# Performance work log

Measured on AMD Instinct MI355X. Metric: run time of the kernel, lower is better.

## Reference

```python
import jax, jax.numpy as jnp
import numpy as np
from jax import lax

GRID = 50
T_DIM = 1
Y_DIM = GRID * GRID
R_DIM = 128
Z_DIM = 64
H_DIM = 128
C_CONV = 32


def _conv(x, w, b):
    # x: [N, Cin, H, W], w: [Cout, Cin, 3, 3]
    y = lax.conv_general_dilated(x, w, (1, 1), 'SAME',
                                 dimension_numbers=('NCHW', 'OIHW', 'NCHW'))
    return y + b[None, :, None, None]


def setup_inputs() -> dict:
    key = jax.random.key(0)
    ks = jax.random.split(key, 24)
    B, NC, NT = 16, 64, 128
    s = lambda k, sh, f: (jax.random.normal(k, sh, jnp.float32) * f)
    inp = {
        'x_context': jax.random.normal(ks[0], (B, NC, T_DIM), jnp.float32),
        'y_context': jax.random.normal(ks[1], (B, NC, Y_DIM), jnp.float32),
        'x_target': jax.random.normal(ks[2], (B, NT, T_DIM), jnp.float32),
        'eps': jax.random.normal(ks[3], (B, Z_DIM), jnp.float32),
        # CNN encoder (Net)
        'w1': s(ks[4], (C_CONV, 2, 3, 3), 0.2), 'b1': jnp.zeros((C_CONV,), jnp.float32),
        'w2': s(ks[5], (C_CONV, C_CONV, 3, 3), 0.1), 'b2': jnp.zeros((C_CONV,), jnp.float32),
        'We1': s(ks[6], (C_CONV + T_DIM, H_DIM), 0.1), 'be1': jnp.zeros((H_DIM,), jnp.float32),
        'We2': s(ks[7], (H_DIM, R_DIM), 0.1), 'be2': jnp.zeros((R_DIM,), jnp.float32),
        # MuSigmaEncoder
        'Wh': s(ks[8], (R_DIM, H_DIM), 0.1), 'bh': jnp.zeros((H_DIM,), jnp.float32),
        'Wmu': s(ks[9], (H_DIM, Z_DIM), 0.1), 'bmu': jnp.zeros((Z_DIM,), jnp.float32),
        'Wsig': s(ks[10], (H_DIM, Z_DIM), 0.1), 'bsig': jnp.zeros((Z_DIM,), jnp.float32),
        # Decoder
        'Wd1': s(ks[11], (T_DIM + Z_DIM, H_DIM), 0.1), 'bd1': jnp.zeros((H_DIM,), jnp.float32),
        'Wd2': s(ks[12], (H_DIM, H_DIM), 0.1), 'bd2': jnp.zeros((H_DIM,), jnp.float32),
        'Wdmu': s(ks[13], (H_DIM, Y_DIM), 0.05), 'bdmu': jnp.zeros((Y_DIM,), jnp.float32),
        'Wdsig': s(ks[14], (H_DIM, Y_DIM), 0.05), 'bdsig': jnp.zeros((Y_DIM,), jnp.float32),
    }
    return inp


def _xy_to_mu_sigma(x, y, p):
    B, N, _ = x.shape
    x_flat = x.reshape(B * N, T_DIM)                      # [BN, 1]
    y_grid = y.reshape(B * N, 1, GRID, GRID)              # [BN,1,50,50]
    # broadcast of x value over the grid (replaces per-sample Python loop)
    x_grid = jnp.broadcast_to(x_flat[:, 0, None, None, None], (B * N, 1, GRID, GRID))
    xy_grid = jnp.concatenate([y_grid, x_grid], axis=1)   # [BN,2,50,50]
    h = jax.nn.relu(_conv(xy_grid, p['w1'], p['b1']))
    h = jax.nn.relu(_conv(h, p['w2'], p['b2']))
    pooled = h.mean(axis=(2, 3))                          # [BN, C_CONV]
    feat = jnp.concatenate([pooled, x_flat], axis=-1)     # [BN, C_CONV+1]
    r_i = jnp.dot(jax.nn.relu(jnp.dot(feat, p['We1']) + p['be1']), p['We2']) + p['be2']
    r = r_i.reshape(B, N, R_DIM).mean(axis=1)             # aggregate over points
    hr = jax.nn.relu(jnp.dot(r, p['Wh']) + p['bh'])
    mu = jnp.dot(hr, p['Wmu']) + p['bmu']
    sigma = 0.1 + 0.9 * jax.nn.sigmoid(jnp.dot(hr, p['Wsig']) + p['bsig'])
    return mu, sigma


def _decode(x_target, z, p):
    B, M, _ = x_target.shape
    z_rep = jnp.broadcast_to(z[:, None, :], (B, M, Z_DIM))
    xz = jnp.concatenate([x_target, z_rep], axis=-1)      # [B,M,1+Z]
    h = jax.nn.relu(jnp.dot(xz, p['Wd1']) + p['bd1'])
    h = jax.nn.relu(jnp.dot(h, p['Wd2']) + p['bd2'])
    y_mu = jnp.dot(h, p['Wdmu']) + p['bdmu']
    y_sigma = 0.1 + 0.9 * jax.nn.softplus(jnp.dot(h, p['Wdsig']) + p['bdsig'])
    return y_mu, y_sigma


def reference(x_context, y_context, x_target, eps,
              w1, b1, w2, b2, We1, be1, We2, be2,
              Wh, bh, Wmu, bmu, Wsig, bsig,
              Wd1, bd1, Wd2, bd2, Wdmu, bdmu, Wdsig, bdsig):
    p = dict(w1=w1, b1=b1, w2=w2, b2=b2, We1=We1, be1=be1, We2=We2, be2=be2,
             Wh=Wh, bh=bh, Wmu=Wmu, bmu=bmu, Wsig=Wsig, bsig=bsig,
             Wd1=Wd1, bd1=bd1, Wd2=Wd2, bd2=bd2, Wdmu=Wdmu, bdmu=bdmu,
             Wdsig=Wdsig, bdsig=bdsig)
    mu_c, sigma_c = _xy_to_mu_sigma(x_context, y_context, p)
    z = mu_c + sigma_c * eps                               # rsample (reparameterized)
    y_mu, y_sigma = _decode(x_target, z, p)
    return y_mu, y_sigma, mu_c, sigma_c
```

## Files before the change

### kernel.cpp

```cpp
#include <hip/hip_runtime.h>

#define GRID_N   50
#define YDIM     2500
#define BATCH    16
#define NCTX     64
#define NTGT     128
#define BN       1024
#define RDIM     128
#define ZDIM     64
#define HDIM     128
#define CCONV    32
#define NSTRIP   5
#define STRIPROWS 10

typedef __attribute__((ext_vector_type(8))) short  s8v;
typedef __attribute__((ext_vector_type(4))) float  f4v;
typedef __attribute__((ext_vector_type(4))) unsigned int u4v;

__device__ __forceinline__ unsigned short f2bf(float f) {
    unsigned int u = __float_as_uint(f);
    u += 0x7FFFu + ((u >> 16) & 1u);
    return (unsigned short)(u >> 16);
}
__device__ __forceinline__ unsigned int cvtpk(float lo, float hi) {
    unsigned int r;
    asm("v_cvt_pk_bf16_f32 %0, %1, %2" : "=v"(r) : "v"(lo), "v"(hi));
    return r;
}


#define PLB   39936
#define PY    2
#define PX    738
#define P1    1490
#define DUP   2228
#define OFFT  48848
#define REDB  48912
#define SMEMB 49424

__global__ void k_pack_w(const float* __restrict__ w1, const float* __restrict__ b1,
                         const float* __restrict__ w2,
                         unsigned short* __restrict__ w2p, unsigned short* __restrict__ w1p)
{
    int t = threadIdx.x;
    int l = t & 63, qq = t >> 6;
    int cout_lo = l & 15, cb = (l >> 4) & 3;
    for (int e = qq; e < 18; e += 4) {
        int tap = e >> 1, ntt = e & 1;
        int cout = ntt * 16 + cout_lo;
        unsigned int pk[4];
#pragma unroll
        for (int g = 0; g < 4; ++g) {
            int cin0 = cb * 8 + 2 * g;
            unsigned int lo = f2bf(w2[(cout * 32 + cin0) * 9 + tap]);
            unsigned int hi = f2bf(w2[(cout * 32 + cin0 + 1) * 9 + tap]);
            pk[g] = lo | (hi << 16);
        }
        uint4 o; o.x = pk[0]; o.y = pk[1]; o.z = pk[2]; o.w = pk[3];
        *(uint4*)&w2p[((tap * 2 + ntt) * 64 + l) * 8] = o;
    }
    if (t < 128) {
        int ct = t >> 6, lane = t & 63;
        int c = ct * 16 + (lane & 15), q2 = lane >> 4;
        const signed char kmap[32] = {0,1,3,4,6,7,16,17,  2,-1,5,-1,8,-1,18,-1,
                                      19,20,21,-1,22,23,24,-1, 32,-1,-1,-1,-1,-1,-1,-1};
        unsigned short v8[8];
#pragma unroll
        for (int j = 0; j < 8; ++j) {
            int km = kmap[q2 * 8 + j];
            float v = 0.f;
            if (km == 32) v = b1[c];
            else if (km >= 16) v = w1[(c * 2 + 1) * 9 + (km - 16)];
            else if (km >= 0) v = w1[(c * 2 + 0) * 9 + km];
            v8[j] = f2bf(v);
        }
        uint4 o;
        o.x = (unsigned)v8[0] | ((unsigned)v8[1] << 16);
        o.y = (unsigned)v8[2] | ((unsigned)v8[3] << 16);
        o.z = (unsigned)v8[4] | ((unsigned)v8[5] << 16);
        o.w = (unsigned)v8[6] | ((unsigned)v8[7] << 16);
        *(uint4*)&w1p[(ct * 64 + lane) * 8] = o;
    }
}

__global__ void k_pack_wd(const float* __restrict__ Wmu, const float* __restrict__ Wsg,
                          unsigned short* __restrict__ wdp)
{
    int nt = blockIdx.x;
    int which = blockIdx.y;
    const float* W = which ? Wsg : Wmu;
    unsigned short* outp = wdp + (size_t)which * (157 * 4 * 64 * 8);
    int t = threadIdx.x;
    int l = t & 63, ks = t >> 6;
    int n = nt * 16 + (l & 15);
    int kbase = ks * 32 + ((l >> 4) & 3) * 8;
    unsigned int pk[4];
#pragma unroll
    for (int g = 0; g < 4; ++g) {
        float f0 = (n < 2500) ? W[(kbase + 2 * g) * 2500 + n] : 0.f;
        float f1 = (n < 2500) ? W[(kbase + 2 * g + 1) * 2500 + n] : 0.f;
        pk[g] = (unsigned int)f2bf(f0) | ((unsigned int)f2bf(f1) << 16);
    }
    uint4 o; o.x = pk[0]; o.y = pk[1]; o.z = pk[2]; o.w = pk[3];
    *(uint4*)&outp[((nt * 4 + ks) * 64 + l) * 8] = o;
}

__global__ __launch_bounds__(256, 3) void k_conv(
    const float* __restrict__ xc, const float* __restrict__ yc,
    const unsigned short* __restrict__ w1p, const unsigned short* __restrict__ w2p,
    const float* __restrict__ b2, float* __restrict__ part)
{
    __shared__ __align__(16) char smem[SMEMB];
    unsigned short* pl = (unsigned short*)(smem + PLB);
    int* offtab = (int*)(smem + OFFT);
    float* redbuf = (float*)(smem + REDB);

    const int t = threadIdx.x, lane = t & 63, w = t >> 6;
    const int l15 = lane & 15, q = lane >> 4;
    const int par = lane & 1;
    const int blk = blockIdx.x, s = blk / NSTRIP, strip = blk - s * NSTRIP;
    const int r0 = strip * STRIPROWS;

    const float xv = xc[s];
    const unsigned short xbf = f2bf(xv);
    const float b2v0 = b2[l15], b2v1 = b2[16 + l15];

    if (t < 16) {
        const int btab[16] = {1, 53, 105, 737,   3, 55, 107, 739,
                              789, 791, 841, 843,  P1, P1, P1, P1};
        offtab[t] = btab[t];
    }
    for (int e = t; e < 736; e += 256) {
        unsigned ry = ((unsigned)(e * 1261)) >> 16;
        int ycol = e - (int)ry * 52;
        int gy = r0 - 2 + (int)ry, gc = ycol - 1;
        bool inb = ((unsigned)gy < 50u) && ((unsigned)gc < 50u);
        unsigned short yb = 0, xb = 0;
        if (inb) { yb = f2bf(yc[s * YDIM + gy * 50 + gc]); xb = xbf; }
        int s0 = PY + e, s1 = PX + e, s2 = P1 + e;
        pl[s0] = yb; if (s0 >= 3) pl[DUP + s0 - 3] = yb;
        pl[s1] = xb; pl[DUP + s1 - 3] = xb;
        pl[s2] = 0x3F80; pl[DUP + s2 - 3] = 0x3F80;
    }
    __syncthreads();

    s8v w1f[2];
#pragma unroll
    for (int ct = 0; ct < 2; ++ct)
        w1f[ct] = *(const s8v*)&w1p[(ct * 64 + lane) * 8];
    int boff[4];
#pragma unroll
    for (int i = 0; i < 4; ++i) {
        int B = offtab[q * 4 + i];
        int pr = (B + lane) & 1;
        boff[i] = PLB + ((pr ? (DUP - 3 + B) : B) << 1);
    }
    const f4v zf = {0.f, 0.f, 0.f, 0.f};
    for (int mt = w; mt < 39; mt += 4) {
        int m = mt * 16 + l15;
        int mb = m * 2;
        unsigned g0 = *(const unsigned*)(smem + boff[0] + mb);
        unsigned g1 = *(const unsigned*)(smem + boff[1] + mb);
        unsigned g2 = *(const unsigned*)(smem + boff[2] + mb);
        unsigned g3 = *(const unsigned*)(smem + boff[3] + mb);
        u4v gg = {g0, g1, g2, g3};
        s8v af = __builtin_bit_cast(s8v, gg);
        f4v c0 = __builtin_amdgcn_mfma_f32_16x16x32_bf16(w1f[0], af, zf, 0, 0, 0);
        f4v c1 = __builtin_amdgcn_mfma_f32_16x16x32_bf16(w1f[1], af, zf, 0, 0, 0);
        unsigned mr = ((unsigned)(m * 1261)) >> 16;
        int mc = m - (int)mr * 52;
        int gy = r0 - 1 + (int)mr;
        bool valid = ((unsigned)(mc - 1) < 50u) && ((unsigned)gy < 50u);
        unsigned p0 = cvtpk(fmaxf(c0[0], 0.f), fmaxf(c0[1], 0.f));
        unsigned p1 = cvtpk(fmaxf(c0[2], 0.f), fmaxf(c0[3], 0.f));
        unsigned p2 = cvtpk(fmaxf(c1[0], 0.f), fmaxf(c1[1], 0.f));
        unsigned p3 = cvtpk(fmaxf(c1[2], 0.f), fmaxf(c1[3], 0.f));
        if (!valid) { p0 = 0u; p1 = 0u; p2 = 0u; p3 = 0u; }
        int rrow = m >> 1;
        int modd4 = (m & 1) << 2;
        int r7 = rrow & 7;
        char* base = smem + (rrow << 7) + ((q & 1) << 3);
        int s0w = ((modd4 | (q >> 1)) ^ r7) << 4;
        int s1w = ((modd4 | (2 + (q >> 1))) ^ r7) << 4;
        *(uint2*)(base + s0w) = make_uint2(p0, p1);
        *(uint2*)(base + s1w) = make_uint2(p2, p3);
    }
    __syncthreads();

    f4v acc[8][2];
#pragma unroll
    for (int i = 0; i < 8; ++i) { acc[i][0] = zf; acc[i][1] = zf; }
    int u_[8], up_[8];
#pragma unroll
    for (int tt = 0; tt < 8; ++tt) {
        int m2 = (w * 8 + tt) * 16 + l15;
        unsigned orr = ((unsigned)(m2 * 1311)) >> 16;
        int pc = m2 + 2 * (int)orr;
        u_[tt] = pc >> 1;
        up_[tt] = u_[tt] + par;
    }
    const int oq  = (par << 2) | q;
    const int oqx = ((par ^ 1) << 2) | q;
#pragma unroll
    for (int tp = 0; tp < 9; ++tp) {
        const int ky = tp / 3, kx = tp % 3;
        s8v b0 = *(const s8v*)&w2p[((tp * 2 + 0) * 64 + lane) * 8];
        s8v b1 = *(const s8v*)&w2p[((tp * 2 + 1) * 64 + lane) * 8];
#pragma unroll
        for (int tt = 0; tt < 8; ++tt) {
            int r = (kx == 1 ? up_[tt] : u_[tt]) + 26 * ky + (kx == 2 ? 1 : 0);
            int so = ((kx == 1 ? oqx : oq) ^ (r & 7)) << 4;
            s8v a = *(const s8v*)(smem + (r << 7) + so);
            acc[tt][0] = __builtin_amdgcn_mfma_f32_16x16x32_bf16(a, b0, acc[tt][0], 0, 0, 0);
            acc[tt][1] = __builtin_amdgcn_mfma_f32_16x16x32_bf16(a, b1, acc[tt][1], 0, 0, 0);
        }
    }
    float ps0 = 0.f, ps1 = 0.f;
#pragma unroll
    for (int tt = 0; tt < 8; ++tt) {
        int mbase = (w * 8 + tt) * 16 + q * 4;
#pragma unroll
        for (int r = 0; r < 4; ++r) {
            if (mbase + r < 500) {
                ps0 += fmaxf(acc[tt][0][r] + b2v0, 0.f);
                ps1 += fmaxf(acc[tt][1][r] + b2v1, 0.f);
            }
        }
    }
    ps0 += __shfl_xor(ps0, 16); ps0 += __shfl_xor(ps0, 32);
    ps1 += __shfl_xor(ps1, 16); ps1 += __shfl_xor(ps1, 32);
    if (lane < 16) {
        redbuf[w * 32 + l15] = ps0;
        redbuf[w * 32 + 16 + l15] = ps1;
    }
    __syncthreads();
    if (t < 32)
        part[(s * NSTRIP + strip) * 32 + t] =
            redbuf[t] + redbuf[32 + t] + redbuf[64 + t] + redbuf[96 + t];
}

__global__ void k_enc(const float* __restrict__ part, const float* __restrict__ xc,
                      const float* __restrict__ We1, const float* __restrict__ be1,
                      const float* __restrict__ We2, const float* __restrict__ be2,
                      float* __restrict__ r_i)
{
    __shared__ float feat[33];
    __shared__ float h[128];
    int s = blockIdx.x, j = threadIdx.x;
    if (j < 32) {
        float v = 0.f;
#pragma unroll
        for (int st = 0; st < NSTRIP; ++st) v += part[(s * NSTRIP + st) * 32 + j];
        feat[j] = v * (1.f / 2500.f);
    }
    if (j == 0) feat[32] = xc[s];
    __syncthreads();
    float a = be1[j];
#pragma unroll 4
    for (int k = 0; k < 33; ++k) a = fmaf(feat[k], We1[k * 128 + j], a);
    h[j] = fmaxf(a, 0.f);
    __syncthreads();
    float r = be2[j];
#pragma unroll 8
    for (int k = 0; k < 128; ++k) r = fmaf(h[k], We2[k * 128 + j], r);
    r_i[s * 128 + j] = r;
}

__global__ void k_ms(const float* __restrict__ r_i,
                     const float* __restrict__ Wh, const float* __restrict__ bh,
                     const float* __restrict__ Wmu, const float* __restrict__ bmu,
                     const float* __restrict__ Wsig, const float* __restrict__ bsig,
                     const float* __restrict__ eps, float* __restrict__ out,
                     float* __restrict__ zbuf)
{
    __shared__ float r[128], hr[128], tmp[2][128];
    int b = blockIdx.x, t = threadIdx.x;
    int j = t & 127, g = t >> 7;
    float acc = 0.f;
#pragma unroll 4
    for (int i = g; i < NCTX; i += 2) acc += r_i[(b * NCTX + i) * 128 + j];
    tmp[g][j] = acc;
    __syncthreads();
    if (g == 0) r[j] = (tmp[0][j] + tmp[1][j]) * (1.f / 64.f);
    __syncthreads();
    float a = (g == 0) ? bh[j] : 0.f;
#pragma unroll 8
    for (int k = g * 64; k < g * 64 + 64; ++k) a = fmaf(r[k], Wh[k * 128 + j], a);
    tmp[g][j] = a;
    __syncthreads();
    if (g == 0) hr[j] = fmaxf(tmp[0][j] + tmp[1][j], 0.f);
    __syncthreads();
    if (j < 64) {
        float m = (g == 0) ? bmu[j] : 0.f, sg = (g == 0) ? bsig[j] : 0.f;
#pragma unroll 8
        for (int k = g * 64; k < g * 64 + 64; ++k) {
            m  = fmaf(hr[k], Wmu[k * 64 + j], m);
            sg = fmaf(hr[k], Wsig[k * 64 + j], sg);
        }
        tmp[g][j] = m; tmp[g][64 + j] = sg;
    }
    __syncthreads();
    if (t < 64) {
        float m  = tmp[0][t] + tmp[1][t];
        float sg = tmp[0][64 + t] + tmp[1][64 + t];
        float sig = 0.1f + 0.9f / (1.f + expf(-sg));
        out[10240000 + b * 64 + t] = m;
        out[10241024 + b * 64 + t] = sig;
        zbuf[b * 64 + t] = m + sig * eps[b * 64 + t];
    }
}

__global__ __launch_bounds__(256) void k_dec1(
    const float* __restrict__ xt, const float* __restrict__ zbuf,
    const float* __restrict__ Wd1, const float* __restrict__ bd1,
    const float* __restrict__ Wd2, const float* __restrict__ bd2,
    unsigned short* __restrict__ h2d)
{
    __shared__ float zsh[64];
    __shared__ float vsh[2][128];
    __shared__ float h1sh[4][128];
    int t = threadIdx.x;
    int j = t & 127, g = t >> 7;
    int r0 = blockIdx.x * 4;
    int b = r0 >> 7;
    if (t < 64) zsh[t] = zbuf[b * 64 + t];
    __syncthreads();
    float v = (g == 0) ? bd1[j] : 0.f;
#pragma unroll 8
    for (int k = g * 32; k < g * 32 + 32; ++k)
        v = fmaf(zsh[k], Wd1[(1 + k) * 128 + j], v);
    vsh[g][j] = v;
    __syncthreads();
    float vv = vsh[0][j] + vsh[1][j];
    float w0 = Wd1[j];
    int ra = r0 + g * 2;
    float x0 = xt[ra], x1 = xt[ra + 1];
    h1sh[g * 2][j]     = fmaxf(fmaf(x0, w0, vv), 0.f);
    h1sh[g * 2 + 1][j] = fmaxf(fmaf(x1, w0, vv), 0.f);
    __syncthreads();
    float bd2j = bd2[j];
    float a0 = bd2j, a1 = bd2j;
#pragma unroll 8
    for (int k = 0; k < 128; ++k) {
        float wv = Wd2[k * 128 + j];
        a0 = fmaf(h1sh[g * 2][k], wv, a0);
        a1 = fmaf(h1sh[g * 2 + 1][k], wv, a1);
    }
    h2d[(size_t)ra * 128 + j]       = f2bf(fmaxf(a0, 0.f));
    h2d[(size_t)(ra + 1) * 128 + j] = f2bf(fmaxf(a1, 0.f));
}

__global__ __launch_bounds__(256) void k_gemm(
    const unsigned short* __restrict__ h2d, const unsigned short* __restrict__ wdp,
    const float* __restrict__ bdmu, const float* __restrict__ bdsg,
    float* __restrict__ out)
{
    __shared__ __align__(16) unsigned short Al[64 * 128];
    int t = threadIdx.x, lane = t & 63, w = t >> 6;
    int m0 = blockIdx.x * 64;
    int which = blockIdx.z;
#pragma unroll
    for (int i = 0; i < 4; ++i) {
        int g = t + i * 256;
        int row = g >> 4, bk = g & 15;
        uint4 v = *(const uint4*)&h2d[(size_t)(m0 + row) * 128 + bk * 8];
        *(uint4*)&Al[row * 128 + ((bk ^ (row & 7)) << 3)] = v;
    }
    __syncthreads();
    int nt = blockIdx.y * 4 + w;
    if (nt < 157) {
        const unsigned short* wp = wdp + (size_t)which * (157 * 4 * 64 * 8);
        s8v bfr[4];
#pragma unroll
        for (int ks = 0; ks < 4; ++ks)
            bfr[ks] = *(const s8v*)&wp[((nt * 4 + ks) * 64 + lane) * 8];
        f4v acc[4];
        {
            f4v zf = {0.f, 0.f, 0.f, 0.f};
#pragma unroll
            for (int mt = 0; mt < 4; ++mt) acc[mt] = zf;
        }
        int lcol = lane & 15, lq = lane >> 4;
#pragma unroll
        for (int mt = 0; mt < 4; ++mt) {
            int mrow = mt * 16 + lcol;
#pragma unroll
            for (int ks = 0; ks < 4; ++ks) {
                int bk = ks * 4 + lq;
                s8v a = *(const s8v*)&Al[mrow * 128 + ((bk ^ (mrow & 7)) << 3)];
                acc[mt] = __builtin_amdgcn_mfma_f32_16x16x32_bf16(a, bfr[ks], acc[mt], 0, 0, 0);
            }
        }
        int col = nt * 16 + lcol;
        if (col < 2500) {
            const float* bp = which ? bdsg : bdmu;
            float bv = bp[col];
            size_t zoff = (size_t)which * 5120000;
#pragma unroll
            for (int mt = 0; mt < 4; ++mt)
#pragma unroll
                for (int r = 0; r < 4; ++r) {
                    int row = m0 + mt * 16 + lq * 4 + r;
                    float vv = acc[mt][r] + bv;
                    if (which) {
                        float sp = fmaxf(vv, 0.f) + log1pf(expf(-fabsf(vv)));
                        vv = 0.1f + 0.9f * sp;
                    }
                    out[zoff + (size_t)row * 2500 + col] = vv;
                }
        }
    }
}

extern "C" void kernel_launch(void* const* d_in, const int* in_sizes, int n_in,
                              void* d_out, int out_size, void* d_ws, size_t ws_size,
                              hipStream_t stream)
{
    const float* xc   = (const float*)d_in[0];
    const float* yc   = (const float*)d_in[1];
    const float* xt   = (const float*)d_in[2];
    const float* eps  = (const float*)d_in[3];
    const float* w1   = (const float*)d_in[4];
    const float* b1   = (const float*)d_in[5];
    const float* w2   = (const float*)d_in[6];
    const float* b2   = (const float*)d_in[7];
    const float* We1  = (const float*)d_in[8];
    const float* be1  = (const float*)d_in[9];
    const float* We2  = (const float*)d_in[10];
    const float* be2  = (const float*)d_in[11];
    const float* Wh   = (const float*)d_in[12];
    const float* bh   = (const float*)d_in[13];
    const float* Wmu  = (const float*)d_in[14];
    const float* bmu  = (const float*)d_in[15];
    const float* Wsig = (const float*)d_in[16];
    const float* bsig = (const float*)d_in[17];
    const float* Wd1  = (const float*)d_in[18];
    const float* bd1  = (const float*)d_in[19];
    const float* Wd2  = (const float*)d_in[20];
    const float* bd2  = (const float*)d_in[21];
    const float* Wdmu = (const float*)d_in[22];
    const float* bdmu = (const float*)d_in[23];
    const float* Wdsg = (const float*)d_in[24];
    const float* bdsg = (const float*)d_in[25];

    float* out = (float*)d_out;
    char* wsb  = (char*)d_ws;
    unsigned short* w2p = (unsigned short*)(wsb + 0);
    unsigned short* wdp = (unsigned short*)(wsb + 18432);
    float* part = (float*)(wsb + 1304576);
    float* r_i  = (float*)(wsb + 1959936);
    float* zbuf = (float*)(wsb + 2484224);
    unsigned short* h2d = (unsigned short*)(wsb + 2488320);
    unsigned short* w1p = (unsigned short*)(wsb + 3012608);

    hipLaunchKernelGGL(k_pack_w, dim3(1), dim3(256), 0, stream, w1, b1, w2, w2p, w1p);
    hipLaunchKernelGGL(k_pack_wd, dim3(157, 2), dim3(256), 0, stream, Wdmu, Wdsg, wdp);
    hipLaunchKernelGGL(k_conv, dim3(BN * NSTRIP), dim3(256), 0, stream,
                       xc, yc, w1p, w2p, b2, part);
    hipLaunchKernelGGL(k_enc, dim3(BN), dim3(128), 0, stream,
                       part, xc, We1, be1, We2, be2, r_i);
    hipLaunchKernelGGL(k_ms, dim3(BATCH), dim3(256), 0, stream,
                       r_i, Wh, bh, Wmu, bmu, Wsig, bsig, eps, out, zbuf);
    hipLaunchKernelGGL(k_dec1, dim3(512), dim3(256), 0, stream,
                       xt, zbuf, Wd1, bd1, Wd2, bd2, h2d);
    hipLaunchKernelGGL(k_gemm, dim3(32, 40, 2), dim3(256), 0, stream,
                       h2d, wdp, bdmu, bdsg, out);
}
```

Baseline: 134.6 us.

## Shrink conv LDS footprint, merge pack kernels, and fuse mu/sigma GEMM launches

Overlays the conv1 staging plane onto the conv1-output buffer so k_conv uses less LDS, allowing four blocks per CU instead of three. The boundary conv1 tiles are computed before a barrier and written after it. The offset table moves into registers, the conv2 phase gets a raised wave priority, and the reduction mask is simplified. The two weight-packing kernels merge into one launch, and the decoder GEMM handles mu and sigma in the same block, halving the grid. The input permutation for w2 packing also changes to match a new 16-byte LDS write layout. The LDS aliasing adds an extra barrier and risks read/write hazards.

```diff
diff --git a/kernel.cpp b/kernel.cpp
--- a/kernel.cpp
+++ b/kernel.cpp
@@ -29,68 +29,68 @@
 }
 
 
-#define PLB   39936
+#define PLB   31024
 #define PY    2
 #define PX    738
 #define P1    1490
 #define DUP   2228
-#define OFFT  48848
-#define REDB  48912
-#define SMEMB 49424
-
-__global__ void k_pack_w(const float* __restrict__ w1, const float* __restrict__ b1,
-                         const float* __restrict__ w2,
-                         unsigned short* __restrict__ w2p, unsigned short* __restrict__ w1p)
+#define SMEMB 39936
+
+
+__global__ void k_pack(const float* __restrict__ w1, const float* __restrict__ b1,
+                       const float* __restrict__ w2,
+                       unsigned short* __restrict__ w2p, unsigned short* __restrict__ w1p,
+                       const float* __restrict__ Wmu, const float* __restrict__ Wsg,
+                       unsigned short* __restrict__ wdp)
 {
     int t = threadIdx.x;
-    int l = t & 63, qq = t >> 6;
-    int cout_lo = l & 15, cb = (l >> 4) & 3;
-    for (int e = qq; e < 18; e += 4) {
-        int tap = e >> 1, ntt = e & 1;
-        int cout = ntt * 16 + cout_lo;
-        unsigned int pk[4];
-#pragma unroll
-        for (int g = 0; g < 4; ++g) {
-            int cin0 = cb * 8 + 2 * g;
-            unsigned int lo = f2bf(w2[(cout * 32 + cin0) * 9 + tap]);
-            unsigned int hi = f2bf(w2[(cout * 32 + cin0 + 1) * 9 + tap]);
-            pk[g] = lo | (hi << 16);
-        }
-        uint4 o; o.x = pk[0]; o.y = pk[1]; o.z = pk[2]; o.w = pk[3];
-        *(uint4*)&w2p[((tap * 2 + ntt) * 64 + l) * 8] = o;
-    }
-    if (t < 128) {
-        int ct = t >> 6, lane = t & 63;
-        int c = ct * 16 + (lane & 15), q2 = lane >> 4;
-        const signed char kmap[32] = {0,1,3,4,6,7,16,17,  2,-1,5,-1,8,-1,18,-1,
-                                      19,20,21,-1,22,23,24,-1, 32,-1,-1,-1,-1,-1,-1,-1};
-        unsigned short v8[8];
-#pragma unroll
-        for (int j = 0; j < 8; ++j) {
-            int km = kmap[q2 * 8 + j];
-            float v = 0.f;
-            if (km == 32) v = b1[c];
-            else if (km >= 16) v = w1[(c * 2 + 1) * 9 + (km - 16)];
-            else if (km >= 0) v = w1[(c * 2 + 0) * 9 + km];
-            v8[j] = f2bf(v);
-        }
-        uint4 o;
-        o.x = (unsigned)v8[0] | ((unsigned)v8[1] << 16);
-        o.y = (unsigned)v8[2] | ((unsigned)v8[3] << 16);
-        o.z = (unsigned)v8[4] | ((unsigned)v8[5] << 16);
-        o.w = (unsigned)v8[6] | ((unsigned)v8[7] << 16);
-        *(uint4*)&w1p[(ct * 64 + lane) * 8] = o;
-    }
-}
-
-__global__ void k_pack_wd(const float* __restrict__ Wmu, const float* __restrict__ Wsg,
-                          unsigned short* __restrict__ wdp)
-{
+    if (blockIdx.y == 2) {
+        if (blockIdx.x != 0) return;
+        int l = t & 63, qq = t >> 6;
+        int cout_lo = l & 15, cb = (l >> 4) & 3;
+        for (int e = qq; e < 18; e += 4) {
+            int tap = e >> 1, ntt = e & 1;
+            int cout = ntt * 16 + cout_lo;
+            unsigned int pk[4];
+#pragma unroll
+            for (int g = 0; g < 4; ++g) {
+                int jj = 2 * g;
+                int cinL = (jj < 4) ? (cb * 4 + jj) : (16 + cb * 4 + (jj - 4));
+                unsigned int lo = f2bf(w2[(cout * 32 + cinL) * 9 + tap]);
+                unsigned int hi = f2bf(w2[(cout * 32 + cinL + 1) * 9 + tap]);
+                pk[g] = lo | (hi << 16);
+            }
+            uint4 o; o.x = pk[0]; o.y = pk[1]; o.z = pk[2]; o.w = pk[3];
+            *(uint4*)&w2p[((tap * 2 + ntt) * 64 + l) * 8] = o;
+        }
+        if (t < 128) {
+            int ct = t >> 6, lane = t & 63;
+            int c = ct * 16 + (lane & 15), q2 = lane >> 4;
+            const signed char kmap[32] = {0,1,3,4,6,7,16,17,  2,-1,5,-1,8,-1,18,-1,
+                                          19,20,21,-1,22,23,24,-1, 32,-1,-1,-1,-1,-1,-1,-1};
+            unsigned short v8[8];
+#pragma unroll
+            for (int j = 0; j < 8; ++j) {
+                int km = kmap[q2 * 8 + j];
+                float v = 0.f;
+                if (km == 32) v = b1[c];
+                else if (km >= 16) v = w1[(c * 2 + 1) * 9 + (km - 16)];
+                else if (km >= 0) v = w1[(c * 2 + 0) * 9 + km];
+                v8[j] = f2bf(v);
+            }
+            uint4 o;
+            o.x = (unsigned)v8[0] | ((unsigned)v8[1] << 16);
+            o.y = (unsigned)v8[2] | ((unsigned)v8[3] << 16);
+            o.z = (unsigned)v8[4] | ((unsigned)v8[5] << 16);
+            o.w = (unsigned)v8[6] | ((unsigned)v8[7] << 16);
+            *(uint4*)&w1p[(ct * 64 + lane) * 8] = o;
+        }
+        return;
+    }
     int nt = blockIdx.x;
     int which = blockIdx.y;
     const float* W = which ? Wsg : Wmu;
     unsigned short* outp = wdp + (size_t)which * (157 * 4 * 64 * 8);
-    int t = threadIdx.x;
     int l = t & 63, ks = t >> 6;
     int n = nt * 16 + (l & 15);
     int kbase = ks * 32 + ((l >> 4) & 3) * 8;
@@ -105,15 +105,14 @@
     *(uint4*)&outp[((nt * 4 + ks) * 64 + l) * 8] = o;
 }
 
-__global__ __launch_bounds__(256, 3) void k_conv(
+__global__ __launch_bounds__(256, 4) void k_conv(
     const float* __restrict__ xc, const float* __restrict__ yc,
     const unsigned short* __restrict__ w1p, const unsigned short* __restrict__ w2p,
     const float* __restrict__ b2, float* __restrict__ part)
 {
     __shared__ __align__(16) char smem[SMEMB];
     unsigned short* pl = (unsigned short*)(smem + PLB);
-    int* offtab = (int*)(smem + OFFT);
-    float* redbuf = (float*)(smem + REDB);
+    float* redbuf = (float*)smem;
 
     const int t = threadIdx.x, lane = t & 63, w = t >> 6;
     const int l15 = lane & 15, q = lane >> 4;
@@ -125,11 +124,6 @@
     const unsigned short xbf = f2bf(xv);
     const float b2v0 = b2[l15], b2v1 = b2[16 + l15];
 
-    if (t < 16) {
-        const int btab[16] = {1, 53, 105, 737,   3, 55, 107, 739,
-                              789, 791, 841, 843,  P1, P1, P1, P1};
-        offtab[t] = btab[t];
-    }
     for (int e = t; e < 736; e += 256) {
         unsigned ry = ((unsigned)(e * 1261)) >> 16;
         int ycol = e - (int)ry * 52;
@@ -142,27 +136,32 @@
         pl[s1] = xb; pl[DUP + s1 - 3] = xb;
         pl[s2] = 0x3F80; pl[DUP + s2 - 3] = 0x3F80;
     }
-    __syncthreads();
 
     s8v w1f[2];
 #pragma unroll
     for (int ct = 0; ct < 2; ++ct)
         w1f[ct] = *(const s8v*)&w1p[(ct * 64 + lane) * 8];
-    int boff[4];
-#pragma unroll
-    for (int i = 0; i < 4; ++i) {
-        int B = offtab[q * 4 + i];
+
+    int B0 = (q == 0) ? 1 : (q == 1) ? 3 : (q == 2) ? 789 : P1;
+    int B1 = (q < 2) ? (B0 + 52)  : ((q == 2) ? 791 : P1);
+    int B2 = (q < 2) ? (B0 + 104) : ((q == 2) ? 841 : P1);
+    int B3 = (q < 2) ? (B0 + 736) : ((q == 2) ? 843 : P1);
+    auto mkoff = [&](int B) {
         int pr = (B + lane) & 1;
-        boff[i] = PLB + ((pr ? (DUP - 3 + B) : B) << 1);
-    }
+        return PLB + ((pr ? (DUP - 3 + B) : B) << 1);
+    };
+    const int bo0 = mkoff(B0), bo1 = mkoff(B1), bo2 = mkoff(B2), bo3 = mkoff(B3);
+
+    __syncthreads();
+
     const f4v zf = {0.f, 0.f, 0.f, 0.f};
-    for (int mt = w; mt < 39; mt += 4) {
+    auto do_tile = [&](int mt) -> uint4 {
         int m = mt * 16 + l15;
         int mb = m * 2;
-        unsigned g0 = *(const unsigned*)(smem + boff[0] + mb);
-        unsigned g1 = *(const unsigned*)(smem + boff[1] + mb);
-        unsigned g2 = *(const unsigned*)(smem + boff[2] + mb);
-        unsigned g3 = *(const unsigned*)(smem + boff[3] + mb);
+        unsigned g0 = *(const unsigned*)(smem + bo0 + mb);
+        unsigned g1 = *(const unsigned*)(smem + bo1 + mb);
+        unsigned g2 = *(const unsigned*)(smem + bo2 + mb);
+        unsigned g3 = *(const unsigned*)(smem + bo3 + mb);
         u4v gg = {g0, g1, g2, g3};
         s8v af = __builtin_bit_cast(s8v, gg);
         f4v c0 = __builtin_amdgcn_mfma_f32_16x16x32_bf16(w1f[0], af, zf, 0, 0, 0);
@@ -176,14 +175,34 @@
         unsigned p2 = cvtpk(fmaxf(c1[0], 0.f), fmaxf(c1[1], 0.f));
         unsigned p3 = cvtpk(fmaxf(c1[2], 0.f), fmaxf(c1[3], 0.f));
         if (!valid) { p0 = 0u; p1 = 0u; p2 = 0u; p3 = 0u; }
+        return make_uint4(p0, p1, p2, p3);
+    };
+    auto wr_tile = [&](int mt, uint4 v) {
+        int m = mt * 16 + l15;
         int rrow = m >> 1;
-        int modd4 = (m & 1) << 2;
-        int r7 = rrow & 7;
-        char* base = smem + (rrow << 7) + ((q & 1) << 3);
-        int s0w = ((modd4 | (q >> 1)) ^ r7) << 4;
-        int s1w = ((modd4 | (2 + (q >> 1))) ^ r7) << 4;
-        *(uint2*)(base + s0w) = make_uint2(p0, p1);
-        *(uint2*)(base + s1w) = make_uint2(p2, p3);
+        int slot = (((m & 1) << 2) | q) ^ (rrow & 7);
+        *(uint4*)(smem + (rrow << 7) + (slot << 4)) = v;
+    };
+
+#pragma unroll
+    for (int it = 0; it < 8; ++it) {
+        int mt = w + it * 4;
+        if (mt <= 29) {
+            uint4 v = do_tile(mt);
+            wr_tile(mt, v);
+        }
+    }
+    {
+        int mt0 = (w >= 2) ? (28 + w) : (32 + w);
+        uint4 hA = do_tile(mt0);
+        uint4 hB = do_tile(mt0 + 4);
+        uint4 hC = make_uint4(0u, 0u, 0u, 0u);
+        bool third = (w == 2);
+        if (third) hC = do_tile(38);
+        __syncthreads();
+        wr_tile(mt0, hA);
+        wr_tile(mt0 + 4, hB);
+        if (third) wr_tile(38, hC);
     }
     __syncthreads();
 
@@ -196,11 +215,14 @@
         int m2 = (w * 8 + tt) * 16 + l15;
         unsigned orr = ((unsigned)(m2 * 1311)) >> 16;
         int pc = m2 + 2 * (int)orr;
-        u_[tt] = pc >> 1;
-        up_[tt] = u_[tt] + par;
+        int u = pc >> 1;
+        u = (u > 258) ? 258 : u;
+        u_[tt] = u;
+        up_[tt] = u + par;
     }
     const int oq  = (par << 2) | q;
     const int oqx = ((par ^ 1) << 2) | q;
+    __builtin_amdgcn_s_setprio(1);
 #pragma unroll
     for (int tp = 0; tp < 9; ++tp) {
         const int ky = tp / 3, kx = tp % 3;
@@ -215,20 +237,32 @@
             acc[tt][1] = __builtin_amdgcn_mfma_f32_16x16x32_bf16(a, b1, acc[tt][1], 0, 0, 0);
         }
     }
+    __builtin_amdgcn_s_setprio(0);
+
     float ps0 = 0.f, ps1 = 0.f;
 #pragma unroll
     for (int tt = 0; tt < 8; ++tt) {
-        int mbase = (w * 8 + tt) * 16 + q * 4;
-#pragma unroll
-        for (int r = 0; r < 4; ++r) {
-            if (mbase + r < 500) {
+        int tile = w * 8 + tt;
+        if (tile != 31) {
+#pragma unroll
+            for (int r = 0; r < 4; ++r) {
                 ps0 += fmaxf(acc[tt][0][r] + b2v0, 0.f);
                 ps1 += fmaxf(acc[tt][1][r] + b2v1, 0.f);
             }
+        } else {
+            int mbase = tile * 16 + q * 4;
+#pragma unroll
+            for (int r = 0; r < 4; ++r) {
+                if (mbase + r < 500) {
+                    ps0 += fmaxf(acc[tt][0][r] + b2v0, 0.f);
+                    ps1 += fmaxf(acc[tt][1][r] + b2v1, 0.f);
+                }
+            }
         }
     }
     ps0 += __shfl_xor(ps0, 16); ps0 += __shfl_xor(ps0, 32);
     ps1 += __shfl_xor(ps1, 16); ps1 += __shfl_xor(ps1, 32);
+    __syncthreads();
     if (lane < 16) {
         redbuf[w * 32 + l15] = ps0;
         redbuf[w * 32 + 16 + l15] = ps1;
@@ -358,7 +392,6 @@
     __shared__ __align__(16) unsigned short Al[64 * 128];
     int t = threadIdx.x, lane = t & 63, w = t >> 6;
     int m0 = blockIdx.x * 64;
-    int which = blockIdx.z;
 #pragma unroll
     for (int i = 0; i < 4; ++i) {
         int g = t + i * 256;
@@ -369,45 +402,48 @@
     __syncthreads();
     int nt = blockIdx.y * 4 + w;
     if (nt < 157) {
-        const unsigned short* wp = wdp + (size_t)which * (157 * 4 * 64 * 8);
-        s8v bfr[4];
-#pragma unroll
-        for (int ks = 0; ks < 4; ++ks)
-            bfr[ks] = *(const s8v*)&wp[((nt * 4 + ks) * 64 + lane) * 8];
-        f4v acc[4];
-        {
-            f4v zf = {0.f, 0.f, 0.f, 0.f};
-#pragma unroll
-            for (int mt = 0; mt < 4; ++mt) acc[mt] = zf;
-        }
         int lcol = lane & 15, lq = lane >> 4;
-#pragma unroll
-        for (int mt = 0; mt < 4; ++mt) {
-            int mrow = mt * 16 + lcol;
-#pragma unroll
-            for (int ks = 0; ks < 4; ++ks) {
-                int bk = ks * 4 + lq;
-                s8v a = *(const s8v*)&Al[mrow * 128 + ((bk ^ (mrow & 7)) << 3)];
-                acc[mt] = __builtin_amdgcn_mfma_f32_16x16x32_bf16(a, bfr[ks], acc[mt], 0, 0, 0);
-            }
-        }
         int col = nt * 16 + lcol;
-        if (col < 2500) {
-            const float* bp = which ? bdsg : bdmu;
-            float bv = bp[col];
-            size_t zoff = (size_t)which * 5120000;
-#pragma unroll
-            for (int mt = 0; mt < 4; ++mt)
-#pragma unroll
-                for (int r = 0; r < 4; ++r) {
-                    int row = m0 + mt * 16 + lq * 4 + r;
-                    float vv = acc[mt][r] + bv;
-                    if (which) {
-                        float sp = fmaxf(vv, 0.f) + log1pf(expf(-fabsf(vv)));
-                        vv = 0.1f + 0.9f * sp;
+#pragma unroll
+        for (int which = 0; which < 2; ++which) {
+            const unsigned short* wp = wdp + (size_t)which * (157 * 4 * 64 * 8);
+            s8v bfr[4];
+#pragma unroll
+            for (int ks = 0; ks < 4; ++ks)
+                bfr[ks] = *(const s8v*)&wp[((nt * 4 + ks) * 64 + lane) * 8];
+            f4v acc[4];
+            {
+                f4v zf = {0.f, 0.f, 0.f, 0.f};
+#pragma unroll
+                for (int mt = 0; mt < 4; ++mt) acc[mt] = zf;
+            }
+#pragma unroll
+            for (int mt = 0; mt < 4; ++mt) {
+                int mrow = mt * 16 + lcol;
+#pragma unroll
+                for (int ks = 0; ks < 4; ++ks) {
+                    int bk = ks * 4 + lq;
+                    s8v a = *(const s8v*)&Al[mrow * 128 + ((bk ^ (mrow & 7)) << 3)];
+                    acc[mt] = __builtin_amdgcn_mfma_f32_16x16x32_bf16(a, bfr[ks], acc[mt], 0, 0, 0);
+                }
+            }
+            if (col < 2500) {
+                const float* bp = which ? bdsg : bdmu;
+                float bv = bp[col];
+                size_t zoff = (size_t)which * 5120000;
+#pragma unroll
+                for (int mt = 0; mt < 4; ++mt)
+#pragma unroll
+                    for (int r = 0; r < 4; ++r) {
+                        int row = m0 + mt * 16 + lq * 4 + r;
+                        float vv = acc[mt][r] + bv;
+                        if (which) {
+                            float sp = fmaxf(vv, 0.f) + log1pf(expf(-fabsf(vv)));
+                            vv = 0.1f + 0.9f * sp;
+                        }
+                        out[zoff + (size_t)row * 2500 + col] = vv;
                     }
-                    out[zoff + (size_t)row * 2500 + col] = vv;
-                }
+            }
         }
     }
 }
@@ -453,8 +489,8 @@
     unsigned short* h2d = (unsigned short*)(wsb + 2488320);
     unsigned short* w1p = (unsigned short*)(wsb + 3012608);
 
-    hipLaunchKernelGGL(k_pack_w, dim3(1), dim3(256), 0, stream, w1, b1, w2, w2p, w1p);
-    hipLaunchKernelGGL(k_pack_wd, dim3(157, 2), dim3(256), 0, stream, Wdmu, Wdsg, wdp);
+    hipLaunchKernelGGL(k_pack, dim3(157, 3), dim3(256), 0, stream,
+                       w1, b1, w2, w2p, w1p, Wdmu, Wdsg, wdp);
     hipLaunchKernelGGL(k_conv, dim3(BN * NSTRIP), dim3(256), 0, stream,
                        xc, yc, w1p, w2p, b2, part);
     hipLaunchKernelGGL(k_enc, dim3(BN), dim3(128), 0, stream,
@@ -463,6 +499,6 @@
                        r_i, Wh, bh, Wmu, bmu, Wsig, bsig, eps, out, zbuf);
     hipLaunchKernelGGL(k_dec1, dim3(512), dim3(256), 0, stream,
                        xt, zbuf, Wd1, bd1, Wd2, bd2, h2d);
-    hipLaunchKernelGGL(k_gemm, dim3(32, 40, 2), dim3(256), 0, stream,
+    hipLaunchKernelGGL(k_gemm, dim3(32, 40), dim3(256), 0, stream,
                        h2d, wdp, bdmu, bdsg, out);
 }
```

New measurement: 118.1 us. 1.14x faster.
